# Kernel optimization log

Measured on AMD Instinct MI355X. Metric: run time of the kernel, lower is better.

The kernel has to match this reference:

```python
import jax, jax.numpy as jnp
import numpy as np

N_NODES = 100000
N_EDGES = 1600000
IN_DIM = 128
HIDDEN = 128
OUT_DIM = 10
N_GRAPHS = 512
N_LAYERS = 3


def setup_inputs() -> dict:
    key = jax.random.key(0)
    ks = jax.random.split(key, 12)
    s_in = 1.0 / np.sqrt(IN_DIM)
    s_h = 1.0 / np.sqrt(HIDDEN)
    return {
        "x": jax.random.normal(ks[0], (N_NODES, IN_DIM), jnp.float32),
        "lin1_w": jax.random.normal(ks[1], (IN_DIM, HIDDEN), jnp.float32) * s_in,
        "lin1_b": jnp.zeros((HIDDEN,), jnp.float32),
        "gcn_w": jax.random.normal(ks[2], (N_LAYERS, HIDDEN, HIDDEN), jnp.float32) * s_h,
        "gcn_b": jnp.zeros((N_LAYERS, HIDDEN), jnp.float32),
        "lin_out_w": jax.random.normal(ks[3], (HIDDEN, HIDDEN), jnp.float32) * s_h,
        "lin_out_b": jnp.zeros((HIDDEN,), jnp.float32),
        "cls_w": jax.random.normal(ks[4], (HIDDEN, OUT_DIM), jnp.float32) * s_h,
        "cls_b": jnp.zeros((OUT_DIM,), jnp.float32),
        "edge_index": jax.random.randint(ks[5], (2, N_EDGES), 0, N_NODES, jnp.int64),
        "batch": jnp.sort(jax.random.randint(ks[6], (N_NODES,), 0, N_GRAPHS, jnp.int64)),
    }


def reference(x, lin1_w, lin1_b, gcn_w, gcn_b, lin_out_w, lin_out_b, cls_w, cls_b, edge_index, batch):
    n = x.shape[0]
    # GCNConv normalization with added self-loops (PyG default)
    row, col = edge_index[0], edge_index[1]
    loop = jnp.arange(n)
    row2 = jnp.concatenate([row, loop])  # source (message origin)
    col2 = jnp.concatenate([col, loop])  # target (aggregation index)
    deg = jax.ops.segment_sum(jnp.ones_like(col2, dtype=x.dtype), col2, num_segments=n)
    dinv = jax.lax.rsqrt(jnp.maximum(deg, 1.0))
    norm = (dinv[row2] * dinv[col2])[:, None]  # [E+N, 1]

    counts = jax.ops.segment_sum(jnp.ones((n,), x.dtype), batch, num_segments=N_GRAPHS)
    counts = jnp.maximum(counts, 1.0)[:, None]

    def readout_mean(h):  # global_mean_pool -> [G, H]
        return jax.ops.segment_sum(h, batch, num_segments=N_GRAPHS) / counts

    # lin1 + elu (dropout = identity in eval mode)
    h = jax.nn.elu(x @ lin1_w + lin1_b)
    reps = readout_mean(h)  # readout_layers[0]; l_sum accumulates layer reps
    for i in range(N_LAYERS):
        hw = h @ gcn_w[i]                       # [N, H]
        msg = norm * hw[row2]                   # gather + scale
        agg = jax.ops.segment_sum(msg, col2, num_segments=n)  # scatter-add
        h = jax.nn.elu(agg + gcn_b[i])          # GCNConv bias then NaOp act
        # pooling op is 'none' (remove_pooling=True): graph unchanged
        reps = reps + readout_mean(h)           # readout_layers[i+1], summed by LaOp 'l_sum'
    g = jax.nn.elu(reps @ lin_out_w + lin_out_b)
    logits = g @ cls_w + cls_b
    return jax.nn.log_softmax(logits, axis=-1)
```

## Files before the change

### kernel.cpp

```cpp
#include <hip/hip_runtime.h>
#include <hip/hip_bf16.h>
#include <math.h>

#define NN 100000
#define NE 1600000
#define HID 128
#define NG 512
#define NB 512
#define RB 196

typedef unsigned short ushort_t;
typedef __attribute__((ext_vector_type(8))) short bf16x8;
typedef __attribute__((ext_vector_type(8))) unsigned short ushort8_t;
typedef __attribute__((ext_vector_type(4))) float f32x4;

__device__ __forceinline__ ushort_t f2bf(float v) {
    unsigned u = __float_as_uint(v);
    unsigned r = (u + 0x7FFF + ((u >> 16) & 1)) >> 16;
    return (ushort_t)r;
}
__device__ __forceinline__ float bf2f(ushort_t u) {
    return __uint_as_float((unsigned)u << 16);
}

__global__ __launch_bounds__(256) void bucket_hist(const int* __restrict__ ecol, int* __restrict__ ghist, int E) {
    __shared__ int lh[NB];
    for (int i = threadIdx.x; i < NB; i += 256) lh[i] = 0;
    __syncthreads();
    for (int e = blockIdx.x * 256 + threadIdx.x; e < E; e += gridDim.x * 256)
        atomicAdd(&lh[ecol[e] / RB], 1);
    __syncthreads();
    for (int i = threadIdx.x; i < NB; i += 256) {
        int c = lh[i];
        if (c) atomicAdd(&ghist[i], c);
    }
}

__global__ __launch_bounds__(NB) void bucket_scan(const int* __restrict__ ghist, int* __restrict__ brp,
                                                  int* __restrict__ gcur, int* __restrict__ rp) {
    __shared__ int s[NB];
    int t = threadIdx.x;
    int v = ghist[t];
    s[t] = v;
    __syncthreads();
    for (int off = 1; off < NB; off <<= 1) {
        int x = (t >= off) ? s[t - off] : 0;
        __syncthreads();
        s[t] += x;
        __syncthreads();
    }
    int ex = s[t] - v;
    brp[t] = ex;
    gcur[t] = ex;
    if (t == NB - 1) { brp[NB] = s[t]; rp[NN] = s[t]; }
}

#define CHUNK 4096
__global__ __launch_bounds__(256) void partition_edges(const int* __restrict__ erow, const int* __restrict__ ecol,
                                                       int* __restrict__ gcur, int2* __restrict__ pairs, int E) {
    __shared__ int cnt[NB];
    __shared__ int base[NB];
    const int t = threadIdx.x;
    const int e0 = blockIdx.x * CHUNK;
    const int e1 = min(e0 + CHUNK, E);
    for (int i = t; i < NB; i += 256) cnt[i] = 0;
    __syncthreads();
    for (int e = e0 + t; e < e1; e += 256) atomicAdd(&cnt[ecol[e] / RB], 1);
    __syncthreads();
    for (int i = t; i < NB; i += 256) {
        int c = cnt[i];
        base[i] = c ? atomicAdd(&gcur[i], c) : 0;
        cnt[i] = 0;
    }
    __syncthreads();
    for (int e = e0 + t; e < e1; e += 256) {
        int d = ecol[e];
        int b = d / RB;
        int off = atomicAdd(&cnt[b], 1);
        pairs[base[b] + off] = make_int2(erow[e], d);
    }
}

__global__ __launch_bounds__(256) void bucket_fill(const int2* __restrict__ pairs, const int* __restrict__ brp,
                                                   int* __restrict__ rp, float* __restrict__ dinv,
                                                   int* __restrict__ csrc) {
    __shared__ int cnt[RB];
    __shared__ int cur[RB];
    __shared__ int sc[256];
    const int b = blockIdx.x, t = threadIdx.x;
    const int nbase = b * RB;
    const int s = brp[b], e = brp[b + 1];
    for (int i = t; i < RB; i += 256) cnt[i] = 0;
    __syncthreads();
    for (int i = s + t; i < e; i += 256) atomicAdd(&cnt[pairs[i].y - nbase], 1);
    __syncthreads();
    int v = (t < RB) ? cnt[t] : 0;
    sc[t] = v;
    __syncthreads();
    for (int off = 1; off < 256; off <<= 1) {
        int x = (t >= off) ? sc[t - off] : 0;
        __syncthreads();
        sc[t] += x;
        __syncthreads();
    }
    if (t < RB) {
        int ex = s + sc[t] - v;
        int node = nbase + t;
        if (node < NN) {
            rp[node] = ex;
            dinv[node] = rsqrtf((float)v + 1.0f);
        }
        cur[t] = ex;
    }
    __syncthreads();
    for (int i = s + t; i < e; i += 256) {
        int2 p = pairs[i];
        int slot = atomicAdd(&cur[p.y - nbase], 1);
        csrc[slot] = p.x;
    }
}

__global__ __launch_bounds__(256) void prep_w(const float* __restrict__ lin1_w,
                                              const float* __restrict__ gcn_w,
                                              ushort_t* __restrict__ wt_hi,
                                              ushort_t* __restrict__ wt_lo) {
    int m = blockIdx.x >> 3;
    int chunk = blockIdx.x & 7;
    const float* W = (m == 0) ? lin1_w : gcn_w + (size_t)(m - 1) * 16384;
    ushort_t* hi = wt_hi + (size_t)m * 16384;
    ushort_t* lo = wt_lo + (size_t)m * 16384;
    for (int i = chunk * 2048 + threadIdx.x; i < (chunk + 1) * 2048; i += 256) {
        int j = i & 7;
        int lane = (i >> 3) & 63;
        int ks = (i >> 9) & 3;
        int ct = (i >> 11) & 7;
        int n = ct * 16 + (lane & 15);
        int k = ks * 32 + (lane >> 4) * 8 + j;
        float v = W[k * 128 + n];
        ushort_t h = f2bf(v);
        hi[i] = h;
        lo[i] = f2bf(v - bf2f(h));
    }
}

template<bool F32A, int MODE>
__global__ __launch_bounds__(256) void gemm_mfma(const float* __restrict__ A,
                                                 const ushort_t* __restrict__ a_bf,
                                                 const ushort_t* __restrict__ wt_hi,
                                                 const ushort_t* __restrict__ wt_lo,
                                                 const float* __restrict__ bias,
                                                 const float* __restrict__ dinv,
                                                 ushort_t* __restrict__ out0,
                                                 int N) {
    const int lane = threadIdx.x & 63;
    const int wid = threadIdx.x >> 6;
    const int rowBase = blockIdx.x * 128 + wid * 32;
    const int l15 = lane & 15, lg = lane >> 4;

    f32x4 acc[2][8];
#pragma unroll
    for (int rt = 0; rt < 2; ++rt)
#pragma unroll
        for (int ct = 0; ct < 8; ++ct) acc[rt][ct] = (f32x4){0.f, 0.f, 0.f, 0.f};

#pragma unroll
    for (int ks = 0; ks < 4; ++ks) {
        bf16x8 ahi[2], alo[2];
#pragma unroll
        for (int rt = 0; rt < 2; ++rt) {
            int r = rowBase + rt * 16 + l15;
            if (F32A) {
                float av[8];
                if (r < N) {
                    const float* ap = A + (size_t)r * 128 + ks * 32 + lg * 8;
                    float4 a0 = *(const float4*)(ap);
                    float4 a1 = *(const float4*)(ap + 4);
                    av[0] = a0.x; av[1] = a0.y; av[2] = a0.z; av[3] = a0.w;
                    av[4] = a1.x; av[5] = a1.y; av[6] = a1.z; av[7] = a1.w;
                } else {
#pragma unroll
                    for (int j = 0; j < 8; ++j) av[j] = 0.f;
                }
#pragma unroll
                for (int j = 0; j < 8; ++j) {
                    ushort_t h = f2bf(av[j]);
                    ahi[rt][j] = (short)h;
                    alo[rt][j] = (short)f2bf(av[j] - bf2f(h));
                }
            } else {
                if (r < N) {
                    ahi[rt] = *(const bf16x8*)(a_bf + (size_t)r * 128 + ks * 32 + lg * 8);
                } else {
                    bf16x8 z = {0, 0, 0, 0, 0, 0, 0, 0};
                    ahi[rt] = z;
                }
            }
        }
#pragma unroll
        for (int ct = 0; ct < 8; ++ct) {
            size_t boff = (size_t)(((ct * 4 + ks) * 64 + lane) * 8);
            bf16x8 bhi = *(const bf16x8*)(wt_hi + boff);
            bf16x8 blo = *(const bf16x8*)(wt_lo + boff);
            acc[0][ct] = __builtin_amdgcn_mfma_f32_16x16x32_bf16(ahi[0], bhi, acc[0][ct], 0, 0, 0);
            acc[1][ct] = __builtin_amdgcn_mfma_f32_16x16x32_bf16(ahi[1], bhi, acc[1][ct], 0, 0, 0);
            acc[0][ct] = __builtin_amdgcn_mfma_f32_16x16x32_bf16(ahi[0], blo, acc[0][ct], 0, 0, 0);
            acc[1][ct] = __builtin_amdgcn_mfma_f32_16x16x32_bf16(ahi[1], blo, acc[1][ct], 0, 0, 0);
            if (F32A) {
                acc[0][ct] = __builtin_amdgcn_mfma_f32_16x16x32_bf16(alo[0], bhi, acc[0][ct], 0, 0, 0);
                acc[1][ct] = __builtin_amdgcn_mfma_f32_16x16x32_bf16(alo[1], bhi, acc[1][ct], 0, 0, 0);
            }
        }
    }

#pragma unroll
    for (int rt = 0; rt < 2; ++rt) {
#pragma unroll
        for (int reg = 0; reg < 4; ++reg) {
            int row = rowBase + rt * 16 + lg * 4 + reg;
            if (row >= N) continue;
            if (MODE == 0) {
#pragma unroll
                for (int ct = 0; ct < 8; ++ct) {
                    int colc = ct * 16 + l15;
                    float v = acc[rt][ct][reg] + bias[colc];
                    v = v > 0.f ? v : expf(v) - 1.f;
                    out0[(size_t)row * 128 + colc] = f2bf(v);
                }
            } else {
                float dv = dinv[row];
#pragma unroll
                for (int ct = 0; ct < 8; ++ct) {
                    int colc = ct * 16 + l15;
                    out0[(size_t)row * 128 + colc] = f2bf(acc[rt][ct][reg] * dv);
                }
            }
        }
    }
}

__global__ __launch_bounds__(256) void gather_agg(const int* __restrict__ rp,
                                                  const int* __restrict__ csrc,
                                                  const float* __restrict__ dinv,
                                                  const ushort_t* __restrict__ hwb,
                                                  const float* __restrict__ bias,
                                                  ushort_t* __restrict__ h_out) {
    int v = blockIdx.x * 16 + (threadIdx.x >> 4);
    if (v >= NN) return;
    int c8 = (threadIdx.x & 15) << 3;
    int s = rp[v], e = rp[v + 1];
    float acc[8] = {};

    int i = s;
    for (; i + 8 <= e; i += 8) {
        int u[8];
#pragma unroll
        for (int k = 0; k < 8; ++k) u[k] = csrc[i + k];
        ushort8_t r[8];
#pragma unroll
        for (int k = 0; k < 8; ++k) r[k] = *(const ushort8_t*)(hwb + (size_t)u[k] * 128 + c8);
#pragma unroll
        for (int k = 0; k < 8; ++k)
#pragma unroll
            for (int j = 0; j < 8; ++j) acc[j] += bf2f(r[k][j]);
    }
    for (; i < e; ++i) {
        int u = csrc[i];
        ushort8_t r0 = *(const ushort8_t*)(hwb + (size_t)u * 128 + c8);
#pragma unroll
        for (int j = 0; j < 8; ++j) acc[j] += bf2f(r0[j]);
    }

    float di = dinv[v];
    ushort8_t sv = *(const ushort8_t*)(hwb + (size_t)v * 128 + c8);
    ushort8_t o;
#pragma unroll
    for (int j = 0; j < 8; ++j) {
        float t = di * (acc[j] + bf2f(sv[j])) + bias[c8 + j];
        t = t > 0.f ? t : expf(t) - 1.f;
        o[j] = f2bf(t);
    }
    *(ushort8_t*)(h_out + (size_t)v * 128 + c8) = o;
}

__global__ __launch_bounds__(128) void readout(const ushort_t* __restrict__ h,
                                               const int* __restrict__ batch,
                                               int n, float* __restrict__ reps) {
    int g = blockIdx.x >> 2;
    int part = blockIdx.x & 3;
    int lo = 0, hi = n;
    while (lo < hi) { int m = (lo + hi) >> 1; if (batch[m] < g) lo = m + 1; else hi = m; }
    int s = lo;
    lo = 0; hi = n;
    while (lo < hi) { int m = (lo + hi) >> 1; if (batch[m] < g + 1) lo = m + 1; else hi = m; }
    int e = lo;
    int c = threadIdx.x;
    float acc = 0.f;
    for (int v = s + part; v < e; v += 4) acc += bf2f(h[(size_t)v * 128 + c]);
    float cnt = (float)(e - s > 0 ? e - s : 1);
    unsafeAtomicAdd(&reps[(size_t)g * 128 + c], acc / cnt);
}

__global__ __launch_bounds__(256) void gemm128(const float* __restrict__ A,
                                               const float* __restrict__ W,
                                               const float* __restrict__ bias,
                                               float* __restrict__ out,
                                               int N, int applyElu) {
    __shared__ float xs[64][128];
    __shared__ float ws[128][64];
    const int tid = threadIdx.x;
    const int rowBase = blockIdx.x * 64;
    const int colBase = blockIdx.y * 64;
#pragma unroll
    for (int it = 0; it < 8; ++it) {
        int idx = it * 256 + tid;
        int r = idx >> 5;
        int c4 = (idx & 31) << 2;
        int gr = rowBase + r;
        float4 v = make_float4(0.f, 0.f, 0.f, 0.f);
        if (gr < N) v = *(const float4*)(A + (size_t)gr * 128 + c4);
        *(float4*)(&xs[r][c4]) = v;
    }
#pragma unroll
    for (int it = 0; it < 8; ++it) {
        int idx = it * 256 + tid;
        int k = idx >> 4;
        int c4 = (idx & 15) << 2;
        *(float4*)(&ws[k][c4]) = *(const float4*)(W + (size_t)k * 128 + colBase + c4);
    }
    __syncthreads();
    const int rowg = tid >> 4, colg = tid & 15;
    const int r0 = rowg * 4, c0 = colg * 4;
    float acc[4][4] = {};
#pragma unroll 2
    for (int kb = 0; kb < 128; kb += 4) {
        float4 xr[4], wr[4];
#pragma unroll
        for (int i = 0; i < 4; ++i) xr[i] = *(const float4*)(&xs[r0 + i][kb]);
#pragma unroll
        for (int kk = 0; kk < 4; ++kk) wr[kk] = *(const float4*)(&ws[kb + kk][c0]);
#pragma unroll
        for (int i = 0; i < 4; ++i) {
            const float* xp = (const float*)&xr[i];
#pragma unroll
            for (int kk = 0; kk < 4; ++kk) {
                float xv = xp[kk];
                acc[i][0] = fmaf(xv, wr[kk].x, acc[i][0]);
                acc[i][1] = fmaf(xv, wr[kk].y, acc[i][1]);
                acc[i][2] = fmaf(xv, wr[kk].z, acc[i][2]);
                acc[i][3] = fmaf(xv, wr[kk].w, acc[i][3]);
            }
        }
    }
    float4 b4 = make_float4(0.f, 0.f, 0.f, 0.f);
    if (bias) b4 = *(const float4*)(bias + colBase + c0);
#pragma unroll
    for (int i = 0; i < 4; ++i) {
        int gr = rowBase + r0 + i;
        if (gr < N) {
            float4 o;
            o.x = acc[i][0] + b4.x;
            o.y = acc[i][1] + b4.y;
            o.z = acc[i][2] + b4.z;
            o.w = acc[i][3] + b4.w;
            if (applyElu) {
                o.x = o.x > 0.f ? o.x : expf(o.x) - 1.f;
                o.y = o.y > 0.f ? o.y : expf(o.y) - 1.f;
                o.z = o.z > 0.f ? o.z : expf(o.z) - 1.f;
                o.w = o.w > 0.f ? o.w : expf(o.w) - 1.f;
            }
            *(float4*)(out + (size_t)gr * 128 + colBase + c0) = o;
        }
    }
}

__global__ __launch_bounds__(64) void cls_logsoftmax(const float* __restrict__ g,
                                                     const float* __restrict__ cw,
                                                     const float* __restrict__ cb,
                                                     float* __restrict__ out) {
    int r = blockIdx.x;
    __shared__ float row[128];
    __shared__ float lg[10];
    int t = threadIdx.x;
    row[t] = g[(size_t)r * 128 + t];
    row[64 + t] = g[(size_t)r * 128 + 64 + t];
    __syncthreads();
    if (t < 10) {
        float a = cb[t];
        for (int k = 0; k < 128; ++k) a = fmaf(row[k], cw[k * 10 + t], a);
        lg[t] = a;
    }
    __syncthreads();
    if (t == 0) {
        float m = lg[0];
#pragma unroll
        for (int j = 1; j < 10; ++j) m = fmaxf(m, lg[j]);
        float se = 0.f;
#pragma unroll
        for (int j = 0; j < 10; ++j) se += expf(lg[j] - m);
        float L = logf(se);
#pragma unroll
        for (int j = 0; j < 10; ++j) out[(size_t)r * 10 + j] = lg[j] - m - L;
    }
}

extern "C" void kernel_launch(void* const* d_in, const int* in_sizes, int n_in,
                              void* d_out, int out_size, void* d_ws, size_t ws_size,
                              hipStream_t stream) {
    const float* x        = (const float*)d_in[0];
    const float* lin1_w   = (const float*)d_in[1];
    const float* lin1_b   = (const float*)d_in[2];
    const float* gcn_w    = (const float*)d_in[3];
    const float* gcn_b    = (const float*)d_in[4];
    const float* lin_out_w= (const float*)d_in[5];
    const float* lin_out_b= (const float*)d_in[6];
    const float* cls_w    = (const float*)d_in[7];
    const float* cls_b    = (const float*)d_in[8];
    const int*   ei       = (const int*)d_in[9];
    const int*   batch    = (const int*)d_in[10];
    float* out = (float*)d_out;

    const int* erow = ei;
    const int* ecol = ei + NE;

    ushort_t* h     = (ushort_t*)d_ws;
    ushort_t* hwb   = h + (size_t)NN * 128;
    float*    dinv  = (float*)(hwb + (size_t)NN * 128);
    float*    reps  = dinv + NN;
    float*    gbuf  = reps + (size_t)NG * 128;
    int*      rp    = (int*)(gbuf + (size_t)NG * 128);
    int*      csrc  = rp + NN + 1;
    int*      ghist = csrc + NE;
    int*      brp   = ghist + NB;
    int*      gcur  = brp + NB + 1;
    ushort_t* wt_hi = (ushort_t*)(gcur + NB);
    ushort_t* wt_lo = wt_hi + 4 * 16384;
    int2*     pairs = (int2*)(wt_lo + 4 * 16384);

    hipMemsetAsync(ghist, 0, NB * sizeof(int), stream);
    hipMemsetAsync(reps, 0, (size_t)NG * 128 * sizeof(float), stream);

    bucket_hist<<<512, 256, 0, stream>>>(ecol, ghist, NE);
    bucket_scan<<<1, NB, 0, stream>>>(ghist, brp, gcur, rp);
    partition_edges<<<(NE + CHUNK - 1) / CHUNK, 256, 0, stream>>>(erow, ecol, gcur, pairs, NE);
    bucket_fill<<<NB, 256, 0, stream>>>(pairs, brp, rp, dinv, csrc);
    prep_w<<<32, 256, 0, stream>>>(lin1_w, gcn_w, wt_hi, wt_lo);

    const int GEMM_GRID = (NN + 127) / 128;

    gemm_mfma<true, 0><<<GEMM_GRID, 256, 0, stream>>>(x, nullptr, wt_hi, wt_lo,
                                                      lin1_b, dinv, h, NN);
    readout<<<NG * 4, 128, 0, stream>>>(h, batch, NN, reps);

    for (int i = 0; i < 3; ++i) {
        gemm_mfma<false, 1><<<GEMM_GRID, 256, 0, stream>>>(nullptr, h,
                                                           wt_hi + (size_t)(i + 1) * 16384,
                                                           wt_lo + (size_t)(i + 1) * 16384,
                                                           nullptr, dinv, hwb, NN);
        gather_agg<<<(NN + 15) / 16, 256, 0, stream>>>(rp, csrc, dinv, hwb,
                                                       gcn_b + (size_t)i * 128, h);
        readout<<<NG * 4, 128, 0, stream>>>(h, batch, NN, reps);
    }

    dim3 gs((NG + 63) / 64, 2);
    gemm128<<<gs, 256, 0, stream>>>(reps, lin_out_w, lin_out_b, gbuf, NG, 1);
    cls_logsoftmax<<<NG, 64, 0, stream>>>(gbuf, cls_w, cls_b, out);
}
```

Measured before the change: 509.0 us.

## Fuse weight prep into histogram, pack edge pairs, widen gather and readout

Merges the weight-prep kernel into the histogram launch as extra blocks, which removes one launch. Edge pairs are packed into 32-bit words (source id shifted left by 8, local destination in the low byte), halving the scratch traffic in partition and fill. The gather loop gains a 16-wide unrolled stage for more loads in flight. Readout now uses 256 threads with 16-byte vector loads and a shared-memory reduction instead of scalar per-column loads. The packing assumes source ids fit in 24 bits and RB fits in 8 bits, and the wider unroll adds register pressure.

```diff
diff --git a/kernel.cpp b/kernel.cpp
--- a/kernel.cpp
+++ b/kernel.cpp
@@ -23,16 +23,41 @@
     return __uint_as_float((unsigned)u << 16);
 }
 
-__global__ __launch_bounds__(256) void bucket_hist(const int* __restrict__ ecol, int* __restrict__ ghist, int E) {
-    __shared__ int lh[NB];
-    for (int i = threadIdx.x; i < NB; i += 256) lh[i] = 0;
-    __syncthreads();
-    for (int e = blockIdx.x * 256 + threadIdx.x; e < E; e += gridDim.x * 256)
-        atomicAdd(&lh[ecol[e] / RB], 1);
-    __syncthreads();
-    for (int i = threadIdx.x; i < NB; i += 256) {
-        int c = lh[i];
-        if (c) atomicAdd(&ghist[i], c);
+__global__ __launch_bounds__(256) void hist_and_prepw(const int* __restrict__ ecol, int* __restrict__ ghist, int E,
+                                                      const float* __restrict__ lin1_w,
+                                                      const float* __restrict__ gcn_w,
+                                                      ushort_t* __restrict__ wt_hi,
+                                                      ushort_t* __restrict__ wt_lo) {
+    if (blockIdx.x < 512) {
+        __shared__ int lh[NB];
+        for (int i = threadIdx.x; i < NB; i += 256) lh[i] = 0;
+        __syncthreads();
+        for (int e = blockIdx.x * 256 + threadIdx.x; e < E; e += 512 * 256)
+            atomicAdd(&lh[ecol[e] / RB], 1);
+        __syncthreads();
+        for (int i = threadIdx.x; i < NB; i += 256) {
+            int c = lh[i];
+            if (c) atomicAdd(&ghist[i], c);
+        }
+    } else {
+        int mb = blockIdx.x - 512;
+        int m = mb >> 3;
+        int chunk = mb & 7;
+        const float* W = (m == 0) ? lin1_w : gcn_w + (size_t)(m - 1) * 16384;
+        ushort_t* hi = wt_hi + (size_t)m * 16384;
+        ushort_t* lo = wt_lo + (size_t)m * 16384;
+        for (int i = chunk * 2048 + threadIdx.x; i < (chunk + 1) * 2048; i += 256) {
+            int j = i & 7;
+            int lane = (i >> 3) & 63;
+            int ks = (i >> 9) & 3;
+            int ct = (i >> 11) & 7;
+            int n = ct * 16 + (lane & 15);
+            int k = ks * 32 + (lane >> 4) * 8 + j;
+            float v = W[k * 128 + n];
+            ushort_t h = f2bf(v);
+            hi[i] = h;
+            lo[i] = f2bf(v - bf2f(h));
+        }
     }
 }
 
@@ -57,7 +82,7 @@
 
 #define CHUNK 4096
 __global__ __launch_bounds__(256) void partition_edges(const int* __restrict__ erow, const int* __restrict__ ecol,
-                                                       int* __restrict__ gcur, int2* __restrict__ pairs, int E) {
+                                                       int* __restrict__ gcur, unsigned int* __restrict__ pairs, int E) {
     __shared__ int cnt[NB];
     __shared__ int base[NB];
     const int t = threadIdx.x;
@@ -77,11 +102,11 @@
         int d = ecol[e];
         int b = d / RB;
         int off = atomicAdd(&cnt[b], 1);
-        pairs[base[b] + off] = make_int2(erow[e], d);
-    }
-}
-
-__global__ __launch_bounds__(256) void bucket_fill(const int2* __restrict__ pairs, const int* __restrict__ brp,
+        pairs[base[b] + off] = ((unsigned)erow[e] << 8) | (unsigned)(d - b * RB);
+    }
+}
+
+__global__ __launch_bounds__(256) void bucket_fill(const unsigned int* __restrict__ pairs, const int* __restrict__ brp,
                                                    int* __restrict__ rp, float* __restrict__ dinv,
                                                    int* __restrict__ csrc) {
     __shared__ int cnt[RB];
@@ -92,7 +117,7 @@
     const int s = brp[b], e = brp[b + 1];
     for (int i = t; i < RB; i += 256) cnt[i] = 0;
     __syncthreads();
-    for (int i = s + t; i < e; i += 256) atomicAdd(&cnt[pairs[i].y - nbase], 1);
+    for (int i = s + t; i < e; i += 256) atomicAdd(&cnt[pairs[i] & 255u], 1);
     __syncthreads();
     int v = (t < RB) ? cnt[t] : 0;
     sc[t] = v;
@@ -114,32 +139,9 @@
     }
     __syncthreads();
     for (int i = s + t; i < e; i += 256) {
-        int2 p = pairs[i];
-        int slot = atomicAdd(&cur[p.y - nbase], 1);
-        csrc[slot] = p.x;
-    }
-}
-
-__global__ __launch_bounds__(256) void prep_w(const float* __restrict__ lin1_w,
-                                              const float* __restrict__ gcn_w,
-                                              ushort_t* __restrict__ wt_hi,
-                                              ushort_t* __restrict__ wt_lo) {
-    int m = blockIdx.x >> 3;
-    int chunk = blockIdx.x & 7;
-    const float* W = (m == 0) ? lin1_w : gcn_w + (size_t)(m - 1) * 16384;
-    ushort_t* hi = wt_hi + (size_t)m * 16384;
-    ushort_t* lo = wt_lo + (size_t)m * 16384;
-    for (int i = chunk * 2048 + threadIdx.x; i < (chunk + 1) * 2048; i += 256) {
-        int j = i & 7;
-        int lane = (i >> 3) & 63;
-        int ks = (i >> 9) & 3;
-        int ct = (i >> 11) & 7;
-        int n = ct * 16 + (lane & 15);
-        int k = ks * 32 + (lane >> 4) * 8 + j;
-        float v = W[k * 128 + n];
-        ushort_t h = f2bf(v);
-        hi[i] = h;
-        lo[i] = f2bf(v - bf2f(h));
+        unsigned int p = pairs[i];
+        int slot = atomicAdd(&cur[p & 255u], 1);
+        csrc[slot] = (int)(p >> 8);
     }
 }
 
@@ -251,6 +253,18 @@
     float acc[8] = {};
 
     int i = s;
+    for (; i + 16 <= e; i += 16) {
+        int u[16];
+#pragma unroll
+        for (int k = 0; k < 16; ++k) u[k] = csrc[i + k];
+        ushort8_t r[16];
+#pragma unroll
+        for (int k = 0; k < 16; ++k) r[k] = *(const ushort8_t*)(hwb + (size_t)u[k] * 128 + c8);
+#pragma unroll
+        for (int k = 0; k < 16; ++k)
+#pragma unroll
+            for (int j = 0; j < 8; ++j) acc[j] += bf2f(r[k][j]);
+    }
     for (; i + 8 <= e; i += 8) {
         int u[8];
 #pragma unroll
@@ -282,7 +296,7 @@
     *(ushort8_t*)(h_out + (size_t)v * 128 + c8) = o;
 }
 
-__global__ __launch_bounds__(128) void readout(const ushort_t* __restrict__ h,
+__global__ __launch_bounds__(256) void readout(const ushort_t* __restrict__ h,
                                                const int* __restrict__ batch,
                                                int n, float* __restrict__ reps) {
     int g = blockIdx.x >> 2;
@@ -293,11 +307,28 @@
     lo = 0; hi = n;
     while (lo < hi) { int m = (lo + hi) >> 1; if (batch[m] < g + 1) lo = m + 1; else hi = m; }
     int e = lo;
-    int c = threadIdx.x;
-    float acc = 0.f;
-    for (int v = s + part; v < e; v += 4) acc += bf2f(h[(size_t)v * 128 + c]);
-    float cnt = (float)(e - s > 0 ? e - s : 1);
-    unsafeAtomicAdd(&reps[(size_t)g * 128 + c], acc / cnt);
+
+    __shared__ float sh[16][128];
+    int ns = threadIdx.x >> 4;
+    int L  = threadIdx.x & 15;
+    int c8 = L << 3;
+    float acc[8] = {};
+    for (int v = s + part + ns * 4; v < e; v += 64) {
+        ushort8_t t = *(const ushort8_t*)(h + (size_t)v * 128 + c8);
+#pragma unroll
+        for (int j = 0; j < 8; ++j) acc[j] += bf2f(t[j]);
+    }
+#pragma unroll
+    for (int j = 0; j < 8; ++j) sh[ns][c8 + j] = acc[j];
+    __syncthreads();
+    if (threadIdx.x < 128) {
+        int c = threadIdx.x;
+        float sum = 0.f;
+#pragma unroll
+        for (int k = 0; k < 16; ++k) sum += sh[k][c];
+        float cnt = (float)(e - s > 0 ? e - s : 1);
+        unsafeAtomicAdd(&reps[(size_t)g * 128 + c], sum / cnt);
+    }
 }
 
 __global__ __launch_bounds__(256) void gemm128(const float* __restrict__ A,
@@ -434,22 +465,21 @@
     int*      gcur  = brp + NB + 1;
     ushort_t* wt_hi = (ushort_t*)(gcur + NB);
     ushort_t* wt_lo = wt_hi + 4 * 16384;
-    int2*     pairs = (int2*)(wt_lo + 4 * 16384);
+    unsigned int* pairs = (unsigned int*)(wt_lo + 4 * 16384);
 
     hipMemsetAsync(ghist, 0, NB * sizeof(int), stream);
     hipMemsetAsync(reps, 0, (size_t)NG * 128 * sizeof(float), stream);
 
-    bucket_hist<<<512, 256, 0, stream>>>(ecol, ghist, NE);
+    hist_and_prepw<<<512 + 32, 256, 0, stream>>>(ecol, ghist, NE, lin1_w, gcn_w, wt_hi, wt_lo);
     bucket_scan<<<1, NB, 0, stream>>>(ghist, brp, gcur, rp);
     partition_edges<<<(NE + CHUNK - 1) / CHUNK, 256, 0, stream>>>(erow, ecol, gcur, pairs, NE);
     bucket_fill<<<NB, 256, 0, stream>>>(pairs, brp, rp, dinv, csrc);
-    prep_w<<<32, 256, 0, stream>>>(lin1_w, gcn_w, wt_hi, wt_lo);
 
     const int GEMM_GRID = (NN + 127) / 128;
 
     gemm_mfma<true, 0><<<GEMM_GRID, 256, 0, stream>>>(x, nullptr, wt_hi, wt_lo,
                                                       lin1_b, dinv, h, NN);
-    readout<<<NG * 4, 128, 0, stream>>>(h, batch, NN, reps);
+    readout<<<NG * 4, 256, 0, stream>>>(h, batch, NN, reps);
 
     for (int i = 0; i < 3; ++i) {
         gemm_mfma<false, 1><<<GEMM_GRID, 256, 0, stream>>>(nullptr, h,
@@ -458,7 +488,7 @@
                                                            nullptr, dinv, hwb, NN);
         gather_agg<<<(NN + 15) / 16, 256, 0, stream>>>(rp, csrc, dinv, hwb,
                                                        gcn_b + (size_t)i * 128, h);
-        readout<<<NG * 4, 128, 0, stream>>>(h, batch, NN, reps);
+        readout<<<NG * 4, 256, 0, stream>>>(h, batch, NN, reps);
     }
 
     dim3 gs((NG + 63) / 64, 2);
```

Result: faster. 455.4 us (-10.5%).
